# Optimization experiments

Measured on AMD Instinct MI355X. Metric: run time of the kernel, lower is better.

## Reference

```python
import jax, jax.numpy as jnp
import numpy as np

H, KV, DH = 16, 4, 64  # num_heads, num_kv_heads, head_dim


def setup_inputs() -> dict:
    key = jax.random.key(0)
    k1, k2, k3, k4, k5 = jax.random.split(key, 5)
    B, L, D = 1, 4096, 1024
    s = 0.02
    return {
        "x": jax.random.normal(k1, (B, L, D), dtype=jnp.float32),
        "Wq": jax.random.normal(k2, (D, H * DH), dtype=jnp.float32) * s,
        "Wk": jax.random.normal(k3, (D, KV * DH), dtype=jnp.float32) * s,
        "Wv": jax.random.normal(k4, (D, KV * DH), dtype=jnp.float32) * s,
        "Wo": jax.random.normal(k5, (H * DH, D), dtype=jnp.float32) * s,
    }


def _rotate_half(t):
    t1, t2 = t[..., : DH // 2], t[..., DH // 2 :]
    return jnp.concatenate([-t2, t1], axis=-1)


def reference(x, Wq, Wk, Wv, Wo):
    B, L, D = x.shape
    G = H // KV  # query heads per kv head
    q = (x @ Wq).reshape(B, L, H, DH)
    k = (x @ Wk).reshape(B, L, KV, DH)
    v = (x @ Wv).reshape(B, L, KV, DH)

    # RoPE: inv_freq over even dims, angles duplicated across both halves
    inv_freq = 1.0 / (10000.0 ** (jnp.arange(0, DH, 2, dtype=jnp.float32) / DH))
    t = jnp.arange(L, dtype=jnp.float32)
    freqs = t[:, None] * inv_freq[None, :]                 # [L, DH/2]
    emb = jnp.concatenate([freqs, freqs], axis=-1)[None, :, None, :]  # [1,L,1,DH]
    cos, sin = jnp.cos(emb), jnp.sin(emb)
    q = q * cos + _rotate_half(q) * sin
    k = k * cos + _rotate_half(k) * sin

    # GQA: query head h attends with kv head h // G (repeat_interleave layout)
    qg = q.reshape(B, L, KV, G, DH)
    scale = DH ** -0.5
    attn = jnp.einsum("bqkgd,bskd->bkgqs", qg, k) * scale  # [B,KV,G,L,L]
    attn = jax.nn.softmax(attn, axis=-1)
    out = jnp.einsum("bkgqs,bskd->bqkgd", attn, v).reshape(B, L, H * DH)
    return out @ Wo
```

## Files before the change

kernel.cpp:

```cpp
#include <hip/hip_runtime.h>
#include <math.h>

#define L 4096
#define D 1024
#define H 16
#define KV 4
#define DH 64

typedef __attribute__((ext_vector_type(8))) short bf16x8;
typedef __attribute__((ext_vector_type(4))) float f32x4;
typedef __attribute__((ext_vector_type(16))) float f32x16;
typedef __attribute__((ext_vector_type(2))) unsigned int u32x2;

static __device__ __forceinline__ unsigned short f2bf(float f) {
    unsigned u = __float_as_uint(f);
    u = (u + 0x7FFF + ((u >> 16) & 1)) >> 16;
    return (unsigned short)u;
}

static __device__ __forceinline__ bf16x8 mk8(unsigned a, unsigned b, unsigned c, unsigned d) {
    union { unsigned u[4]; bf16x8 v; } x;
    x.u[0] = a; x.u[1] = b; x.u[2] = c; x.u[3] = d;
    return x.v;
}

#define EXP2F(x) __builtin_amdgcn_exp2f(x)
#define ZERO16 ((f32x16){0.f,0.f,0.f,0.f,0.f,0.f,0.f,0.f,0.f,0.f,0.f,0.f,0.f,0.f,0.f,0.f})

#define GLD16(src, dst) \
    __builtin_amdgcn_global_load_lds((__attribute__((address_space(1))) void*)(src), \
                                     (__attribute__((address_space(3))) void*)(dst), 16, 0, 0)

__global__ __launch_bounds__(256) void prep_kernel(
        const float* __restrict__ x,  const float* __restrict__ Wq,
        const float* __restrict__ Wk, const float* __restrict__ Wv,
        const float* __restrict__ Wo,
        unsigned short* __restrict__ xb, unsigned short* __restrict__ WqkvT,
        unsigned short* __restrict__ WoT) {
    const int b = blockIdx.x, tid = threadIdx.x;
    if (b < 4096) {
        int i = (b * 256 + tid) * 4;
        float4 v = *(const float4*)&x[i];
        ushort4 o;
        o.x = f2bf(v.x); o.y = f2bf(v.y); o.z = f2bf(v.z); o.w = f2bf(v.w);
        *(ushort4*)&xb[i] = o;
        return;
    }
    __shared__ float t[32][33];
    const float* src; unsigned short* dst; int N, n0, k0;
    if (b < 5120)      { int tq = b - 4096; src = Wq; dst = WqkvT;                     N = 1024; n0 = (tq & 31) * 32; k0 = (tq >> 5) * 32; }
    else if (b < 5376) { int tq = b - 5120; src = Wk; dst = WqkvT + (size_t)1024*1024; N = 256;  n0 = (tq & 7)  * 32; k0 = (tq >> 3) * 32; }
    else if (b < 5632) { int tq = b - 5376; src = Wv; dst = WqkvT + (size_t)1280*1024; N = 256;  n0 = (tq & 7)  * 32; k0 = (tq >> 3) * 32; }
    else               { int tq = b - 5632; src = Wo; dst = WoT;                       N = 1024; n0 = (tq & 31) * 32; k0 = (tq >> 5) * 32; }
    const int tx = tid & 31, ty = tid >> 5;
    #pragma unroll
    for (int j = 0; j < 4; ++j)
        t[ty + 8 * j][tx] = src[(size_t)(k0 + ty + 8 * j) * N + n0 + tx];
    __syncthreads();
    #pragma unroll
    for (int j = 0; j < 4; ++j)
        dst[(size_t)(n0 + ty + 8 * j) * 1024 + k0 + tx] = f2bf(t[tx][ty + 8 * j]);
}

__global__ __launch_bounds__(256) void gemm_bf16(const unsigned short* __restrict__ A,
                                                 const unsigned short* __restrict__ BT,
                                                 float* __restrict__ C,
                                                 int M, int N, int K) {
    __shared__ unsigned short As[128 * 32];
    __shared__ unsigned short Bs[128 * 32];

    const int tid  = threadIdx.x;
    const int w    = tid >> 6;
    const int lane = tid & 63;
    const int c    = lane & 15;
    const int quad = lane >> 4;
    const int wy = w >> 1, wx = w & 1;
    const int row0 = blockIdx.y * 128;
    const int col0 = blockIdx.x * 128;

    const int ld_row = w * 16 + (lane >> 2);
    const int ld_col = (lane & 3) * 8;

    f32x4 acc[4][4];
    #pragma unroll
    for (int mt = 0; mt < 4; ++mt)
        #pragma unroll
        for (int nt = 0; nt < 4; ++nt)
            acc[mt][nt] = (f32x4){0.f, 0.f, 0.f, 0.f};

    for (int k0 = 0; k0 < K; k0 += 32) {
        __syncthreads();
        GLD16(&A [(size_t)(row0 + ld_row)      * K + k0 + ld_col], &As[w * 512]);
        GLD16(&A [(size_t)(row0 + ld_row + 64) * K + k0 + ld_col], &As[w * 512 + 2048]);
        GLD16(&BT[(size_t)(col0 + ld_row)      * K + k0 + ld_col], &Bs[w * 512]);
        GLD16(&BT[(size_t)(col0 + ld_row + 64) * K + k0 + ld_col], &Bs[w * 512 + 2048]);
        __syncthreads();

        bf16x8 af[4], bfr[4];
        #pragma unroll
        for (int mt = 0; mt < 4; ++mt)
            af[mt] = *(const bf16x8*)&As[(wy * 64 + mt * 16 + c) * 32 + quad * 8];
        #pragma unroll
        for (int nt = 0; nt < 4; ++nt)
            bfr[nt] = *(const bf16x8*)&Bs[(wx * 64 + nt * 16 + c) * 32 + quad * 8];

        #pragma unroll
        for (int mt = 0; mt < 4; ++mt)
            #pragma unroll
            for (int nt = 0; nt < 4; ++nt)
                acc[mt][nt] = __builtin_amdgcn_mfma_f32_16x16x32_bf16(af[mt], bfr[nt], acc[mt][nt], 0, 0, 0);
    }

    #pragma unroll
    for (int mt = 0; mt < 4; ++mt)
        #pragma unroll
        for (int nt = 0; nt < 4; ++nt)
            #pragma unroll
            for (int r = 0; r < 4; ++r)
                C[(size_t)(row0 + wy * 64 + mt * 16 + quad * 4 + r) * N
                  + col0 + wx * 64 + nt * 16 + c] = acc[mt][nt][r];
}

__global__ __launch_bounds__(256) void gemm_qkv_rope(
        const unsigned short* __restrict__ A,
        const unsigned short* __restrict__ BT,
        unsigned short* __restrict__ qb,
        unsigned short* __restrict__ kbuf,
        unsigned short* __restrict__ vbuf) {
    __shared__ unsigned short As[128 * 32];
    __shared__ unsigned short Bs[128 * 32];

    const int tid  = threadIdx.x;
    const int w    = tid >> 6;
    const int lane = tid & 63;
    const int c    = lane & 15;
    const int quad = lane >> 4;
    const int wy = w >> 1, wx = w & 1;
    const int row0 = blockIdx.y * 128;
    const int col0 = blockIdx.x * 128;

    const int ld_row = w * 16 + (lane >> 2);
    const int ld_col = (lane & 3) * 8;

    f32x4 acc[4][4];
    #pragma unroll
    for (int mt = 0; mt < 4; ++mt)
        #pragma unroll
        for (int nt = 0; nt < 4; ++nt)
            acc[mt][nt] = (f32x4){0.f, 0.f, 0.f, 0.f};

    for (int k0 = 0; k0 < 1024; k0 += 32) {
        __syncthreads();
        GLD16(&A [(size_t)(row0 + ld_row)      * 1024 + k0 + ld_col], &As[w * 512]);
        GLD16(&A [(size_t)(row0 + ld_row + 64) * 1024 + k0 + ld_col], &As[w * 512 + 2048]);
        GLD16(&BT[(size_t)(col0 + ld_row)      * 1024 + k0 + ld_col], &Bs[w * 512]);
        GLD16(&BT[(size_t)(col0 + ld_row + 64) * 1024 + k0 + ld_col], &Bs[w * 512 + 2048]);
        __syncthreads();

        bf16x8 af[4], bfr[4];
        #pragma unroll
        for (int mt = 0; mt < 4; ++mt)
            af[mt] = *(const bf16x8*)&As[(wy * 64 + mt * 16 + c) * 32 + quad * 8];
        #pragma unroll
        for (int nt = 0; nt < 4; ++nt)
            bfr[nt] = *(const bf16x8*)&Bs[(wx * 64 + nt * 16 + c) * 32 + quad * 8];

        #pragma unroll
        for (int mt = 0; mt < 4; ++mt)
            #pragma unroll
            for (int nt = 0; nt < 4; ++nt)
                acc[mt][nt] = __builtin_amdgcn_mfma_f32_16x16x32_bf16(af[mt], bfr[nt], acc[mt][nt], 0, 0, 0);
    }

    const int colb = col0 + wx * 64;
    if (colb < 1280) {
        unsigned short* dst; int hh, hstride; float scale;
        if (colb < 1024) { dst = qb;   hh = colb >> 6;          hstride = H;  scale = 0.18033688011112042f; }
        else             { dst = kbuf; hh = (colb - 1024) >> 6; hstride = KV; scale = 1.0f; }
        #pragma unroll
        for (int nt = 0; nt < 2; ++nt) {
            int d = nt * 16 + c;
            float invf = EXP2F((float)d * -0.4152410118609203f);
            #pragma unroll
            for (int mt = 0; mt < 4; ++mt)
                #pragma unroll
                for (int r = 0; r < 4; ++r) {
                    int l = row0 + wy * 64 + mt * 16 + quad * 4 + r;
                    float ang = (float)l * invf;
                    float sn = __sinf(ang), cs = __cosf(ang);
                    float x1 = acc[mt][nt][r], x2 = acc[mt][nt + 2][r];
                    dst[((size_t)l * hstride + hh) * DH + d]      = f2bf((x1 * cs - x2 * sn) * scale);
                    dst[((size_t)l * hstride + hh) * DH + d + 32] = f2bf((x2 * cs + x1 * sn) * scale);
                }
        }
    } else {
        int vh = (colb - 1280) >> 6;
        #pragma unroll
        for (int mt = 0; mt < 4; ++mt)
            #pragma unroll
            for (int nt = 0; nt < 4; ++nt)
                #pragma unroll
                for (int r = 0; r < 4; ++r) {
                    int l = row0 + wy * 64 + mt * 16 + quad * 4 + r;
                    vbuf[((size_t)l * KV + vh) * DH + nt * 16 + c] = f2bf(acc[mt][nt][r]);
                }
    }
}

__global__ __attribute__((amdgpu_flat_work_group_size(512, 512), amdgpu_waves_per_eu(2)))
void attn_mfma_kernel(
        const unsigned short* __restrict__ qb,
        const unsigned short* __restrict__ kb,
        const unsigned short* __restrict__ vb,
        unsigned short* __restrict__ ob) {
    __shared__ __align__(16) unsigned short Vt[2][2][64][64];
    __shared__ __align__(16) float Ep[4][64][64];
    __shared__ __align__(16) float Rs[8][2][32];

    const int tid  = threadIdx.x;
    const int w    = tid >> 6;
    const int lane = tid & 63;
    const int c32  = lane & 31;
    const int hi   = lane >> 5;
    const int g    = w >> 2;
    const int kv = blockIdx.y;
    const int h  = kv * 4 + (w & 3);
    const int q0 = blockIdx.x * 64;
    const int s_base = g * 2048;

    bf16x8 qf[2][4];
    {
        const unsigned short* qbase = qb + ((size_t)(q0 + c32) * H + h) * DH + hi * 8;
        #pragma unroll
        for (int qt = 0; qt < 2; ++qt)
            #pragma unroll
            for (int kd = 0; kd < 4; ++kd)
                qf[qt][kd] = *(const bf16x8*)&qbase[qt * 32 * H * DH + kd * 16];
    }

    f32x16 oacc[2][2];
    #pragma unroll
    for (int qt = 0; qt < 2; ++qt)
        #pragma unroll
        for (int dt = 0; dt < 2; ++dt)
            oacc[qt][dt] = ZERO16;
    float rsum[2] = {0.f, 0.f};

    const int tid8 = tid & 255;
    const int sp = tid8 & 31, dc = tid8 >> 5;

    const unsigned short* kbase = kb + ((size_t)(s_base + c32) * KV + kv) * DH + hi * 8;
    const unsigned short* vbase = vb + ((size_t)(s_base + 2 * sp) * KV + kv) * DH + dc * 8;
    unsigned short* VtW = &Vt[g][0][0][0];

    int4 vreg0 = *(const int4*)&vbase[0];
    int4 vreg1 = *(const int4*)&vbase[KV * DH];
    bf16x8 kf[2][4];
    #pragma unroll
    for (int a = 0; a < 2; ++a)
        #pragma unroll
        for (int kd = 0; kd < 4; ++kd)
            kf[a][kd] = *(const bf16x8*)&kbase[a * 32 * KV * DH + kd * 16];

    for (int it = 0; it < 32; ++it) {
        const int bufo = (it & 1) * (64 * 64);

        {
            const unsigned* pa = (const unsigned*)&vreg0;
            const unsigned* pb = (const unsigned*)&vreg1;
            #pragma unroll
            for (int t = 0; t < 4; ++t) {
                unsigned lo = __builtin_amdgcn_perm(pb[t], pa[t], 0x05040100u);
                unsigned hv = __builtin_amdgcn_perm(pb[t], pa[t], 0x07060302u);
                int dl = dc * 8 + 2 * t, dh2 = dl + 1;
                *(unsigned*)&VtW[bufo + dl  * 64 + (((sp >> 2) ^ (dl  & 7)) << 3) + 2 * (sp & 3)] = lo;
                *(unsigned*)&VtW[bufo + dh2 * 64 + (((sp >> 2) ^ (dh2 & 7)) << 3) + 2 * (sp & 3)] = hv;
            }
        }
        __syncthreads();

        const int itn = (it + 1) & 31;
        vreg0 = *(const int4*)&vbase[(size_t)itn * 64 * KV * DH];
        vreg1 = *(const int4*)&vbase[(size_t)itn * 64 * KV * DH + KV * DH];

        #pragma unroll
        for (int kt2 = 0; kt2 < 2; ++kt2) {
            bf16x8 pf[2][2];
            #pragma unroll
            for (int qt = 0; qt < 2; ++qt) {
                f32x16 s = ZERO16;
                #pragma unroll
                for (int kd = 0; kd < 4; ++kd)
                    s = __builtin_amdgcn_mfma_f32_32x32x16_bf16(kf[kt2][kd], qf[qt][kd], s, 0, 0, 0);
                float p[16];
                #pragma unroll
                for (int r = 0; r < 16; ++r)
                    p[r] = __uint_as_float(__float_as_uint(EXP2F(s[r])) & 0xFFFF0000u);
                float t0 = (p[0] + p[1]) + (p[2] + p[3]);
                float t1 = (p[4] + p[5]) + (p[6] + p[7]);
                float t2 = (p[8] + p[9]) + (p[10] + p[11]);
                float t3 = (p[12] + p[13]) + (p[14] + p[15]);
                rsum[qt] += (t0 + t1) + (t2 + t3);
                unsigned u[8];
                #pragma unroll
                for (int i = 0; i < 8; ++i)
                    u[i] = __builtin_amdgcn_perm(__float_as_uint(p[2 * i + 1]),
                                                 __float_as_uint(p[2 * i]), 0x07060302u);
                #pragma unroll
                for (int f = 0; f < 2; ++f) {
                    u32x2 e0 = __builtin_amdgcn_permlane32_swap(u[4 * f + 0], u[4 * f + 2], false, false);
                    u32x2 e1 = __builtin_amdgcn_permlane32_swap(u[4 * f + 1], u[4 * f + 3], false, false);
                    pf[qt][f] = mk8(e0.x, e1.x, e0.y, e1.y);
                }
            }
            if (kt2 == 1) {
                #pragma unroll
                for (int a = 0; a < 2; ++a)
                    #pragma unroll
                    for (int kd = 0; kd < 4; ++kd)
                        kf[a][kd] = *(const bf16x8*)&kbase[((size_t)itn * 64 + a * 32) * KV * DH + kd * 16];
            }
            __builtin_amdgcn_s_setprio(1);
            #pragma unroll
            for (int dt = 0; dt < 2; ++dt)
                #pragma unroll
                for (int f = 0; f < 2; ++f) {
                    bf16x8 vf = *(const bf16x8*)&VtW[bufo + (dt * 32 + c32) * 64
                                    + ((((kt2 * 4 + f * 2 + hi) ^ (c32 & 7)) << 3))];
                    #pragma unroll
                    for (int qt = 0; qt < 2; ++qt)
                        oacc[qt][dt] = __builtin_amdgcn_mfma_f32_32x32x16_bf16(pf[qt][f], vf, oacc[qt][dt], 0, 0, 0);
                }
            __builtin_amdgcn_s_setprio(0);
        }
    }

    #pragma unroll
    for (int qt = 0; qt < 2; ++qt) {
        u32x2 e = __builtin_amdgcn_permlane32_swap(__float_as_uint(rsum[qt]),
                                                   __float_as_uint(rsum[qt]), false, false);
        float tot = __uint_as_float(e.x) + __uint_as_float(e.y);
        Rs[w][qt][c32] = tot;
    }
    if (g == 1) {
        #pragma unroll
        for (int qt = 0; qt < 2; ++qt)
            #pragma unroll
            for (int dt = 0; dt < 2; ++dt) {
                const int d = dt * 32 + c32;
                #pragma unroll
                for (int rr = 0; rr < 4; ++rr) {
                    const int gq = (qt * 8 + 2 * rr + hi) ^ (d & 15);
                    f32x4 val = {oacc[qt][dt][rr * 4 + 0], oacc[qt][dt][rr * 4 + 1],
                                 oacc[qt][dt][rr * 4 + 2], oacc[qt][dt][rr * 4 + 3]};
                    *(f32x4*)&Ep[w - 4][d][gq * 4] = val;
                }
            }
    }
    __syncthreads();
    if (g == 0) {
        #pragma unroll
        for (int qt = 0; qt < 2; ++qt)
            #pragma unroll
            for (int dt = 0; dt < 2; ++dt) {
                const int d = dt * 32 + c32;
                #pragma unroll
                for (int rr = 0; rr < 4; ++rr) {
                    const int gq = (qt * 8 + 2 * rr + hi) ^ (d & 15);
                    f32x4 val = *(const f32x4*)&Ep[w][d][gq * 4];
                    oacc[qt][dt][rr * 4 + 0] += val[0];
                    oacc[qt][dt][rr * 4 + 1] += val[1];
                    oacc[qt][dt][rr * 4 + 2] += val[2];
                    oacc[qt][dt][rr * 4 + 3] += val[3];
                }
            }
        #pragma unroll
        for (int qt = 0; qt < 2; ++qt)
            #pragma unroll
            for (int rr = 0; rr < 4; ++rr) {
                f32x4 ra = *(const f32x4*)&Rs[w][qt][8 * rr + 4 * hi];
                f32x4 rb = *(const f32x4*)&Rs[w + 4][qt][8 * rr + 4 * hi];
                #pragma unroll
                for (int i = 0; i < 4; ++i) {
                    float inv = 1.0f / (ra[i] + rb[i]);
                    int row = q0 + qt * 32 + 8 * rr + 4 * hi + i;
                    #pragma unroll
                    for (int dt = 0; dt < 2; ++dt)
                        ob[(size_t)row * (H * DH) + h * DH + dt * 32 + c32] =
                            f2bf(oacc[qt][dt][rr * 4 + i] * inv);
                }
            }
    }
}

extern "C" void kernel_launch(void* const* d_in, const int* in_sizes, int n_in,
                              void* d_out, int out_size, void* d_ws, size_t ws_size,
                              hipStream_t stream) {
    const float* x  = (const float*)d_in[0];
    const float* Wq = (const float*)d_in[1];
    const float* Wk = (const float*)d_in[2];
    const float* Wv = (const float*)d_in[3];
    const float* Wo = (const float*)d_in[4];
    float* out = (float*)d_out;

    char* ws = (char*)d_ws;
    unsigned short* xb    = (unsigned short*)ws;
    unsigned short* ob    = xb;
    unsigned short* qb    = (unsigned short*)(ws + 8388608);
    unsigned short* kb    = (unsigned short*)(ws + 16777216);
    unsigned short* vb    = (unsigned short*)(ws + 18874368);
    unsigned short* WqkvT = (unsigned short*)(ws + 20971520);
    unsigned short* WoT   = (unsigned short*)(ws + 24117248);

    dim3 blk(256);

    prep_kernel<<<6656, blk, 0, stream>>>(x, Wq, Wk, Wv, Wo, xb, WqkvT, WoT);

    gemm_qkv_rope<<<dim3(12, 32), blk, 0, stream>>>(xb, WqkvT, qb, kb, vb);

    attn_mfma_kernel<<<dim3(L / 64, KV), dim3(512), 0, stream>>>(qb, kb, vb, ob);

    gemm_bf16<<<dim3(D / 128, L / 128), blk, 0, stream>>>(ob, WoT, out, L, D, D);
}
```

Measured before the change: 213.6 us.

## Store V transposed from QKV GEMM and load attention V fragments directly from global

The QKV GEMM epilogue now writes V in a transposed [kv*DH, L] layout using 4-wide vector stores. The attention kernel then loads V MFMA fragments straight from global memory into registers. This removes the per-iteration shared-memory transpose, the Vt LDS buffer and a __syncthreads. In exchange, V loads are no longer prefetched one iteration ahead, so global latency sits directly in front of the PV MFMAs, and register pressure rises.

```diff
diff --git a/kernel.cpp b/kernel.cpp
--- a/kernel.cpp
+++ b/kernel.cpp
@@ -126,7 +126,7 @@
         const unsigned short* __restrict__ BT,
         unsigned short* __restrict__ qb,
         unsigned short* __restrict__ kbuf,
-        unsigned short* __restrict__ vbuf) {
+        unsigned short* __restrict__ vbT) {
     __shared__ unsigned short As[128 * 32];
     __shared__ unsigned short Bs[128 * 32];
 
@@ -196,14 +196,15 @@
     } else {
         int vh = (colb - 1280) >> 6;
         #pragma unroll
-        for (int mt = 0; mt < 4; ++mt)
-            #pragma unroll
-            for (int nt = 0; nt < 4; ++nt)
-                #pragma unroll
-                for (int r = 0; r < 4; ++r) {
-                    int l = row0 + wy * 64 + mt * 16 + quad * 4 + r;
-                    vbuf[((size_t)l * KV + vh) * DH + nt * 16 + c] = f2bf(acc[mt][nt][r]);
-                }
+        for (int nt = 0; nt < 4; ++nt)
+            #pragma unroll
+            for (int mt = 0; mt < 4; ++mt) {
+                int l = row0 + wy * 64 + mt * 16 + quad * 4;
+                ushort4 o;
+                o.x = f2bf(acc[mt][nt][0]); o.y = f2bf(acc[mt][nt][1]);
+                o.z = f2bf(acc[mt][nt][2]); o.w = f2bf(acc[mt][nt][3]);
+                *(ushort4*)&vbT[(size_t)(vh * DH + nt * 16 + c) * L + l] = o;
+            }
     }
 }
 
@@ -211,9 +212,8 @@
 void attn_mfma_kernel(
         const unsigned short* __restrict__ qb,
         const unsigned short* __restrict__ kb,
-        const unsigned short* __restrict__ vb,
+        const unsigned short* __restrict__ vbT,
         unsigned short* __restrict__ ob) {
-    __shared__ __align__(16) unsigned short Vt[2][2][64][64];
     __shared__ __align__(16) float Ep[4][64][64];
     __shared__ __align__(16) float Rs[8][2][32];
 
@@ -246,15 +246,9 @@
             oacc[qt][dt] = ZERO16;
     float rsum[2] = {0.f, 0.f};
 
-    const int tid8 = tid & 255;
-    const int sp = tid8 & 31, dc = tid8 >> 5;
-
-    const unsigned short* kbase = kb + ((size_t)(s_base + c32) * KV + kv) * DH + hi * 8;
-    const unsigned short* vbase = vb + ((size_t)(s_base + 2 * sp) * KV + kv) * DH + dc * 8;
-    unsigned short* VtW = &Vt[g][0][0][0];
-
-    int4 vreg0 = *(const int4*)&vbase[0];
-    int4 vreg1 = *(const int4*)&vbase[KV * DH];
+    const unsigned short* kbase  = kb  + ((size_t)(s_base + c32) * KV + kv) * DH + hi * 8;
+    const unsigned short* vTbase = vbT + (size_t)(kv * DH) * L + s_base + hi * 8;
+
     bf16x8 kf[2][4];
     #pragma unroll
     for (int a = 0; a < 2; ++a)
@@ -263,25 +257,15 @@
             kf[a][kd] = *(const bf16x8*)&kbase[a * 32 * KV * DH + kd * 16];
 
     for (int it = 0; it < 32; ++it) {
-        const int bufo = (it & 1) * (64 * 64);
-
-        {
-            const unsigned* pa = (const unsigned*)&vreg0;
-            const unsigned* pb = (const unsigned*)&vreg1;
-            #pragma unroll
-            for (int t = 0; t < 4; ++t) {
-                unsigned lo = __builtin_amdgcn_perm(pb[t], pa[t], 0x05040100u);
-                unsigned hv = __builtin_amdgcn_perm(pb[t], pa[t], 0x07060302u);
-                int dl = dc * 8 + 2 * t, dh2 = dl + 1;
-                *(unsigned*)&VtW[bufo + dl  * 64 + (((sp >> 2) ^ (dl  & 7)) << 3) + 2 * (sp & 3)] = lo;
-                *(unsigned*)&VtW[bufo + dh2 * 64 + (((sp >> 2) ^ (dh2 & 7)) << 3) + 2 * (sp & 3)] = hv;
-            }
-        }
-        __syncthreads();
+        bf16x8 vfrag[2][4];
+        #pragma unroll
+        for (int dt = 0; dt < 2; ++dt)
+            #pragma unroll
+            for (int ck = 0; ck < 4; ++ck)
+                vfrag[dt][ck] = *(const bf16x8*)&vTbase[(size_t)(dt * 32 + c32) * L
+                                                        + it * 64 + ck * 16];
 
         const int itn = (it + 1) & 31;
-        vreg0 = *(const int4*)&vbase[(size_t)itn * 64 * KV * DH];
-        vreg1 = *(const int4*)&vbase[(size_t)itn * 64 * KV * DH + KV * DH];
 
         #pragma unroll
         for (int kt2 = 0; kt2 < 2; ++kt2) {
@@ -325,8 +309,7 @@
             for (int dt = 0; dt < 2; ++dt)
                 #pragma unroll
                 for (int f = 0; f < 2; ++f) {
-                    bf16x8 vf = *(const bf16x8*)&VtW[bufo + (dt * 32 + c32) * 64
-                                    + ((((kt2 * 4 + f * 2 + hi) ^ (c32 & 7)) << 3))];
+                    bf16x8 vf = vfrag[dt][kt2 * 2 + f];
                     #pragma unroll
                     for (int qt = 0; qt < 2; ++qt)
                         oacc[qt][dt] = __builtin_amdgcn_mfma_f32_32x32x16_bf16(pf[qt][f], vf, oacc[qt][dt], 0, 0, 0);
@@ -408,7 +391,7 @@
     unsigned short* ob    = xb;
     unsigned short* qb    = (unsigned short*)(ws + 8388608);
     unsigned short* kb    = (unsigned short*)(ws + 16777216);
-    unsigned short* vb    = (unsigned short*)(ws + 18874368);
+    unsigned short* vbT   = (unsigned short*)(ws + 18874368);
     unsigned short* WqkvT = (unsigned short*)(ws + 20971520);
     unsigned short* WoT   = (unsigned short*)(ws + 24117248);
 
@@ -416,9 +399,9 @@
 
     prep_kernel<<<6656, blk, 0, stream>>>(x, Wq, Wk, Wv, Wo, xb, WqkvT, WoT);
 
-    gemm_qkv_rope<<<dim3(12, 32), blk, 0, stream>>>(xb, WqkvT, qb, kb, vb);
-
-    attn_mfma_kernel<<<dim3(L / 64, KV), dim3(512), 0, stream>>>(qb, kb, vb, ob);
+    gemm_qkv_rope<<<dim3(12, 32), blk, 0, stream>>>(xb, WqkvT, qb, kb, vbT);
+
+    attn_mfma_kernel<<<dim3(L / 64, KV), dim3(512), 0, stream>>>(qb, kb, vbT, ob);
 
     gemm_bf16<<<dim3(D / 128, L / 128), blk, 0, stream>>>(ob, WoT, out, L, D, D);
 }
```

Measured after the change: 256.1 us. 1.2x slower.
